# Optimization experiments

Measured on AMD Instinct MI355X. Metric: run time of the kernel, lower is better.

The kernel has to match this reference:

```python
import jax, jax.numpy as jnp
import numpy as np
import math

E = 65536        # neighbor pairs (edges)
NAT = 2048       # atoms
NRAD = 24        # radial basis size
ZETA = [1, 2, 3, 4]
NCOMP = len(ZETA) + 1  # radial components: one 2-body + one per zeta
RCUT = 6.0
NELEM = 94       # one-hot element encoding size
EMB = 16         # species embedding dim


def _tables():
    """Static lxlylz enumeration per zeta: triples with lx+ly+lz = n, n in 0..z,
    multinomial/binomial normalization and (-1)^n lambda sign."""
    f = np.vectorize(math.factorial)
    tabs = []
    for z in ZETA:
        L = []
        for n in range(z + 1):
            for lx in range(n + 1):
                for ly in range(n - lx + 1):
                    L.append((lx, ly, n - lx - ly))
        L = np.array(L, np.int64)              # [K,3]
        nsum = L.sum(1)                        # [K]
        fact_lxlylz = f(L[:, 0]) * f(L[:, 1]) * f(L[:, 2])
        # (nfact/fact_lxlylz) * z!/((z-n)! n!) = z! / ((z-n)! * lx!ly!lz!)
        fact_norm = math.factorial(z) / (f(z - nsum) * fact_lxlylz)
        lam = (-1.0) ** nsum
        tabs.append((jnp.asarray(L, jnp.float32),
                     jnp.asarray(fact_norm, jnp.float32),
                     jnp.asarray(lam, jnp.float32)))
    return tabs

TABS = _tables()


def _forward(rij, Wr1, br1, Wr2, br2, Ws1, bs1, Ws2, bs2,
             Wa1, ba1, Wa2, ba2, Wa3, ba3, first_atom_idx, species_idx):
    nat = species_idx.shape[0]
    r = jnp.linalg.norm(rij, axis=1)                       # [E]
    u = rij / r[:, None]                                   # [E,3] unit vectors
    fc = 0.5 * (jnp.cos(jnp.pi * jnp.minimum(r, RCUT) / RCUT) + 1.0)
    centers = jnp.linspace(0.0, RCUT, NRAD, dtype=jnp.float32)
    width = RCUT / NRAD
    basis = jnp.exp(-((r[:, None] - centers) ** 2) / (2.0 * width * width)) * fc[:, None]  # [E,NRAD]
    # learned radial functions -> [E, NRAD, NCOMP]
    h = jax.nn.silu(basis @ Wr1 + br1)
    radial = jax.nn.silu(h @ Wr2 + br2).reshape(-1, NRAD, NCOMP)
    seg = first_atom_idx
    # two-body descriptor
    feats = [jax.ops.segment_sum(radial[:, :, 0], seg, num_segments=nat)]  # [nat,NRAD]
    for iz, z in enumerate(ZETA):
        L, fnorm, lam = TABS[iz]
        # g_ij over lxlylz combos: prod of powers of unit-vector components
        g_ij = jnp.prod((u[:, None, :] + 1e-12) ** L[None, :, :], axis=-1) * fnorm  # [E,K]
        g = jnp.einsum('er,ek->erk', radial[:, :, iz + 1], g_ij)                    # [E,NRAD,K]
        gi = jax.ops.segment_sum(g, seg, num_segments=nat)                          # [nat,NRAD,K]
        g2 = gi * gi
        norm = 2.0 ** (1.0 - z)
        feats.append(jnp.sum(g2, axis=-1) * norm)          # lambda = +1
        feats.append(jnp.sum(g2 * lam, axis=-1) * norm)    # lambda = -1
    feat = jnp.concatenate(feats, axis=1)                  # [nat, NRAD*(1+2*nzeta)]
    # species embedding and correlation
    onehot = jax.nn.one_hot(species_idx, NELEM, dtype=feat.dtype)
    emb = jax.nn.silu(onehot @ Ws1 + bs1) @ Ws2 + bs2      # [nat,EMB]
    x = (feat[:, :, None] * emb[:, None, :]).reshape(nat, -1)  # [nat, F*EMB]
    h = jax.nn.silu(x @ Wa1 + ba1)
    h = jax.nn.silu(h @ Wa2 + ba2)
    e = h @ Wa3 + ba3                                      # [nat,1] atomic energies
    return jnp.sum(e)                                      # total energy


def setup_inputs() -> dict:
    key = jax.random.key(0)
    ks = jax.random.split(key, 12)
    def w(k, shp):
        return jax.random.normal(k, shp, jnp.float32) / np.float32(np.sqrt(shp[0]))
    F = NRAD * (1 + 2 * len(ZETA)) * EMB  # 3456
    return {
        "rij": jax.random.normal(ks[0], (E, 3), jnp.float32) * 2.0,
        "Wr1": w(ks[1], (NRAD, 64)), "br1": jnp.zeros((64,), jnp.float32),
        "Wr2": w(ks[2], (64, NCOMP * NRAD)), "br2": jnp.zeros((NCOMP * NRAD,), jnp.float32),
        "Ws1": w(ks[3], (NELEM, 32)), "bs1": jnp.zeros((32,), jnp.float32),
        "Ws2": w(ks[4], (32, EMB)), "bs2": jnp.zeros((EMB,), jnp.float32),
        "Wa1": w(ks[5], (F, 256)), "ba1": jnp.zeros((256,), jnp.float32),
        "Wa2": w(ks[6], (256, 128)), "ba2": jnp.zeros((128,), jnp.float32),
        "Wa3": w(ks[7], (128, 1)), "ba3": jnp.zeros((1,), jnp.float32),
        "first_atom_idx": jnp.sort(jax.random.randint(ks[8], (E,), 0, NAT)),
        "species_idx": jax.random.randint(ks[9], (NAT,), 0, NELEM),
    }


def reference(rij, Wr1, br1, Wr2, br2, Ws1, bs1, Ws2, bs2,
              Wa1, ba1, Wa2, ba2, Wa3, ba3, first_atom_idx, species_idx):
    return _forward(rij, Wr1, br1, Wr2, br2, Ws1, bs1, Ws2, bs2,
                    Wa1, ba1, Wa2, ba2, Wa3, ba3, first_atom_idx, species_idx)
```

## Files before the change

### kernel.cpp

```cpp
#include <hip/hip_runtime.h>
#include <math.h>

#define KTOT 69
#define NRADC 24
#define NFEAT 216
#define NELEMC 94
#define EMBC 16
#define H1C 256
#define H2C 128
#define CE 16
#define EPR 20
#define KGN 18
#define GSTR 84
#define GISTR 76

__device__ __constant__ int c_lx[KTOT] = {
  0,0,0,1,
  0,0,0,1,0,0,0,1,1,2,
  0,0,0,1,0,0,0,1,1,2,0,0,0,0,1,1,1,2,2,3,
  0,0,0,1,0,0,0,1,1,2,0,0,0,0,1,1,1,2,2,3,0,0,0,0,0,1,1,1,1,2,2,2,3,3,4};
__device__ __constant__ int c_ly[KTOT] = {
  0,0,1,0,
  0,0,1,0,0,1,2,0,1,0,
  0,0,1,0,0,1,2,0,1,0,0,1,2,3,0,1,2,0,1,0,
  0,0,1,0,0,1,2,0,1,0,0,1,2,3,0,1,2,0,1,0,0,1,2,3,4,0,1,2,3,0,1,2,0,1,0};
__device__ __constant__ int c_lz[KTOT] = {
  0,1,0,0,
  0,1,0,0,2,1,0,1,0,0,
  0,1,0,0,2,1,0,1,0,0,3,2,1,0,2,1,0,1,0,0,
  0,1,0,0,2,1,0,1,0,0,3,2,1,0,2,1,0,1,0,0,4,3,2,1,0,3,2,1,0,2,1,0,1,0,0};
__device__ __constant__ float c_fn[KTOT] = {
  1,1,1,1,
  1,2,2,2,1,2,1,2,2,1,
  1,3,3,3,3,6,3,6,6,3,1,3,3,1,3,6,3,3,3,1,
  1,4,4,4,6,12,6,12,12,6,4,12,12,4,12,24,12,12,12,4,
  1,4,6,4,1,4,12,12,4,6,12,6,4,4,1};
__device__ __constant__ float c_lam[KTOT] = {
  1,-1,-1,-1,
  1,-1,-1,-1,1,1,1,1,1,1,
  1,-1,-1,-1,1,1,1,1,1,1,-1,-1,-1,-1,-1,-1,-1,-1,-1,-1,
  1,-1,-1,-1,1,1,1,1,1,1,-1,-1,-1,-1,-1,-1,-1,-1,-1,-1,
  1,1,1,1,1,1,1,1,1,1,1,1,1,1,1};
__device__ __constant__ int c_k0[4] = {0,4,14,34};
__device__ __constant__ int c_kn[4] = {4,10,20,35};
__device__ __constant__ float c_zn[4] = {1.0f, 0.5f, 0.25f, 0.125f};
__device__ __constant__ int c_zidg[KGN] = {0, 1,1,1, 2,2,2,2,2, 3,3,3,3,3,3,3,3,3};

__device__ __forceinline__ float silu(float x) { return x / (1.0f + expf(-x)); }
__device__ __forceinline__ float4 silu4(float4 v) {
  v.x = silu(v.x); v.y = silu(v.y); v.z = silu(v.z); v.w = silu(v.w); return v;
}
__device__ __forceinline__ void fma4(float4& a, float s, const float4 w) {
  a.x += s * w.x; a.y += s * w.y; a.z += s * w.z; a.w += s * w.w;
}
__device__ __forceinline__ void fma44(float4& a, const float4 x, const float4 y) {
  a.x += x.x * y.x; a.y += x.y * y.y; a.z += x.z * y.z; a.w += x.w * y.w;
}
__device__ __forceinline__ float hsum4(const float4 v) { return (v.x + v.y) + (v.z + v.w); }
__device__ __forceinline__ float powsel(int l, float p, float p2, float p3, float p4) {
  float v = 1.0f;
  v = l >= 1 ? p : v;
  v = l >= 2 ? p2 : v;
  v = l >= 3 ? p3 : v;
  v = l >= 4 ? p4 : v;
  return v;
}

__global__ __launch_bounds__(256) void k_prep(
    const int* __restrict__ fai, const int* __restrict__ spc,
    const float* __restrict__ Ws1, const float* __restrict__ bs1,
    const float* __restrict__ Ws2, const float* __restrict__ bs2,
    const float* __restrict__ Wa1,
    int* __restrict__ bounds, int* __restrict__ order,
    float* __restrict__ B, int E, int nat, int nbB) {
  const int blk = blockIdx.x;
  const int tid = threadIdx.x;
  __shared__ float s_hh[NELEMC * 32];
  __shared__ float s_emb[NELEMC * EMBC];
  __shared__ int s_cnt[NELEMC];
  __shared__ int s_off[NELEMC];

  if (blk < nbB) {
    int e = blk * 256 + tid;
    if (e < E) {
      int f = fai[e];
      int fp = (e == 0) ? -1 : fai[e - 1];
      for (int a = fp + 1; a <= f; ++a) bounds[a] = e;
      if (e == E - 1)
        for (int a = f + 1; a <= nat; ++a) bounds[a] = E;
    }
  } else if (blk == nbB) {
    for (int i = tid; i < NELEMC; i += 256) s_cnt[i] = 0;
    __syncthreads();
    for (int a = tid; a < nat; a += 256) atomicAdd(&s_cnt[spc[a]], 1);
    __syncthreads();
    if (tid == 0) {
      int run = 0;
      for (int s = 0; s < NELEMC; ++s) { s_off[s] = run; run += s_cnt[s]; }
    }
    __syncthreads();
    for (int a = tid; a < nat; a += 256) {
      int pos = atomicAdd(&s_off[spc[a]], 1);
      order[pos] = a;
    }
  } else {
    const int i = blk - nbB - 1;
    const int o = tid;
    for (int idx = tid; idx < NELEMC * 32; idx += 256) {
      int s = idx >> 5, c = idx & 31;
      s_hh[idx] = silu(Ws1[s * 32 + c] + bs1[c]);
    }
    __syncthreads();
    for (int idx = tid; idx < NELEMC * EMBC; idx += 256) {
      int s = idx >> 4, j = idx & 15;
      float acc = bs2[j];
      #pragma unroll
      for (int c = 0; c < 32; ++c) acc += s_hh[s * 32 + c] * Ws2[c * EMBC + j];
      s_emb[idx] = acc;
    }
    __syncthreads();
    float w[EMBC];
    #pragma unroll
    for (int j = 0; j < EMBC; ++j) w[j] = Wa1[(size_t)(i * EMBC + j) * H1C + o];
    for (int s = 0; s < NELEMC; ++s) {
      float acc = 0.0f;
      #pragma unroll
      for (int j = 0; j < EMBC; ++j) acc += s_emb[s * EMBC + j] * w[j];
      B[((size_t)s * NFEAT + i) * H1C + o] = acc;
    }
  }
}

template <int NQ>
__device__ __forceinline__ void edge_l2(
    const float* __restrict__ s_h, const float* __restrict__ Wr2,
    const float* __restrict__ br2, float4* __restrict__ radial4,
    int lane, int og, int ebase, int E) {
  float4 a0[NQ], a1[NQ];
  const float4* b2 = (const float4*)(br2 + og * 32);
  #pragma unroll
  for (int q = 0; q < NQ; ++q) { a0[q] = b2[q]; a1[q] = b2[q]; }
  #pragma unroll 2
  for (int j = 0; j < 64; ++j) {
    float h0 = s_h[lane * 65 + j];
    float h1 = s_h[(lane + 64) * 65 + j];
    const float4* w = (const float4*)(Wr2 + j * 120 + og * 32);
    #pragma unroll
    for (int q = 0; q < NQ; ++q) {
      float4 wq = w[q];
      fma4(a0[q], h0, wq);
      fma4(a1[q], h1, wq);
    }
  }
  const int e0 = ebase + lane, e1 = e0 + 64;
  if (e0 < E) {
    #pragma unroll
    for (int q = 0; q < NQ; ++q) radial4[e0 * 30 + og * 8 + q] = silu4(a0[q]);
  }
  if (e1 < E) {
    #pragma unroll
    for (int q = 0; q < NQ; ++q) radial4[e1 * 30 + og * 8 + q] = silu4(a1[q]);
  }
}

__global__ __launch_bounds__(256) void k_edge(
    const float* __restrict__ rij,
    const float* __restrict__ Wr1, const float* __restrict__ br1,
    const float* __restrict__ Wr2, const float* __restrict__ br2,
    float4* __restrict__ radial4, int E) {
  __shared__ float s_bas[128 * 25];
  __shared__ float s_h[128 * 65];
  const int tid = threadIdx.x;
  const int lane = tid & 63;
  const int og = __builtin_amdgcn_readfirstlane(tid >> 6);
  const int ebase = blockIdx.x * 128;

  {
    const int ehh = og >> 1;
    const int m0 = (og & 1) * 12;
    const int el = ehh * 64 + lane;
    const int eg = ebase + el;
    float x = 0.0f, y = 0.0f, z = 0.0f;
    const bool ev = eg < E;
    if (ev) { x = rij[3 * eg]; y = rij[3 * eg + 1]; z = rij[3 * eg + 2]; }
    float r = sqrtf(x * x + y * y + z * z);
    float fcv = ev ? 0.5f * (cosf(3.14159265358979323846f * fminf(r, 6.0f) *
                                  (1.0f / 6.0f)) + 1.0f)
                   : 0.0f;
    #pragma unroll
    for (int t = 0; t < 12; ++t) {
      int m = m0 + t;
      float d = r - (6.0f / 23.0f) * (float)m;
      s_bas[el * 25 + m] = expf(-8.0f * d * d) * fcv;
    }
  }
  __syncthreads();

  {
    const float4* b1 = (const float4*)(br1 + og * 16);
    float4 c0[4], c1[4];
    #pragma unroll
    for (int q = 0; q < 4; ++q) { c0[q] = b1[q]; c1[q] = b1[q]; }
    #pragma unroll 4
    for (int m = 0; m < NRADC; ++m) {
      float bA = s_bas[lane * 25 + m];
      float bB = s_bas[(lane + 64) * 25 + m];
      const float4* w = (const float4*)(Wr1 + m * 64 + og * 16);
      #pragma unroll
      for (int q = 0; q < 4; ++q) {
        float4 wq = w[q];
        fma4(c0[q], bA, wq);
        fma4(c1[q], bB, wq);
      }
    }
    #pragma unroll
    for (int q = 0; q < 4; ++q) {
      float4 v0 = silu4(c0[q]), v1 = silu4(c1[q]);
      int b0 = lane * 65 + og * 16 + 4 * q;
      int b1o = (lane + 64) * 65 + og * 16 + 4 * q;
      s_h[b0 + 0] = v0.x; s_h[b0 + 1] = v0.y; s_h[b0 + 2] = v0.z; s_h[b0 + 3] = v0.w;
      s_h[b1o + 0] = v1.x; s_h[b1o + 1] = v1.y; s_h[b1o + 2] = v1.z; s_h[b1o + 3] = v1.w;
    }
  }
  __syncthreads();

  if (og < 3) edge_l2<8>(s_h, Wr2, br2, radial4, lane, og, ebase, E);
  else        edge_l2<6>(s_h, Wr2, br2, radial4, lane, og, ebase, E);
}

__global__ __launch_bounds__(256) void k_atom(
    const float* __restrict__ rij,
    const float4* __restrict__ radial4,
    const int* __restrict__ bounds,
    float* __restrict__ feat, int E) {
  const int a = blockIdx.x;
  const int tid = threadIdx.x;
  __shared__ __align__(16) float s_radT[120 * EPR];
  __shared__ __align__(16) float s_gijT[KGN * GSTR];
  __shared__ __align__(16) float s_gi[NRADC * GISTR];
  __shared__ float s_feat[NFEAT];

  const int start = bounds[a];
  const int end = bounds[a + 1];

  const int e = tid & 15;
  const int sub = tid >> 4;

  const bool is_tile = tid < 216;
  const int eh = (tid < 216) ? (tid / 108) : 0;
  const int tile = (tid < 216) ? (tid % 108) : 0;
  const int rg = tile % 6;
  const int kg = tile / 6;
  const int comp0 = rg * 20 + 1 + c_zidg[kg];
  const bool is_2b = (tid >= 216 && tid < 240);
  const int rad2b = tid - 216;

  const int kstart = sub < 5 ? sub * 5 : 25 + (sub - 5) * 4;
  const int kcnt = sub < 5 ? 5 : 4;
  int t_pk[5], t_addr[5]; float t_fn[5];
  #pragma unroll
  for (int t = 0; t < 5; ++t) {
    int k = (t < kcnt) ? kstart + t : 0;
    t_pk[t] = c_lx[k] | (c_ly[k] << 8) | (c_lz[k] << 16);
    t_fn[t] = c_fn[k];
    int prow = k + (k < 14 ? 0 : 2);
    t_addr[t] = (prow >> 2) * GSTR + (prow & 3) * EPR + e;
  }

  const int pe0 = tid / 30, pc0 = tid - pe0 * 30;
  const int pe1 = (tid + 256) / 30, pc1 = (tid + 256) - pe1 * 30;

  if (tid < 60) {
    int rr = tid / EPR, ec = tid % EPR;
    int fkg = rr < 2 ? 3 : 17;
    int fj = rr < 2 ? 2 + rr : 3;
    s_gijT[fkg * GSTR + fj * EPR + ec] = 0.0f;
  }

  float4 acc[4][4];
  #pragma unroll
  for (int i = 0; i < 4; ++i)
    #pragma unroll
    for (int j = 0; j < 4; ++j) acc[i][j] = make_float4(0, 0, 0, 0);
  float4 acc2b = make_float4(0, 0, 0, 0);

  float4 pfA, pfB;
  float rx, ry, rz;
  auto prefetch = [&](int c0) {
    int lim = (end - c0) * 30;
    pfA = make_float4(0, 0, 0, 0);
    pfB = make_float4(0, 0, 0, 0);
    if (tid < lim) pfA = radial4[(size_t)c0 * 30 + tid];
    if (tid < 224 && tid + 256 < lim) pfB = radial4[(size_t)c0 * 30 + 256 + tid];
    int eg = c0 + e;
    rx = 0.0f; ry = 0.0f; rz = 0.0f;
    if (eg < end) { rx = rij[3 * eg]; ry = rij[3 * eg + 1]; rz = rij[3 * eg + 2]; }
  };
  prefetch(start);

  for (int c0 = start; c0 < end; c0 += CE) {
    __syncthreads();
    {
      int c = pc0 * 4;
      s_radT[(c + 0) * EPR + pe0] = pfA.x;
      s_radT[(c + 1) * EPR + pe0] = pfA.y;
      s_radT[(c + 2) * EPR + pe0] = pfA.z;
      s_radT[(c + 3) * EPR + pe0] = pfA.w;
      if (tid < 224) {
        int c2 = pc1 * 4;
        s_radT[(c2 + 0) * EPR + pe1] = pfB.x;
        s_radT[(c2 + 1) * EPR + pe1] = pfB.y;
        s_radT[(c2 + 2) * EPR + pe1] = pfB.z;
        s_radT[(c2 + 3) * EPR + pe1] = pfB.w;
      }
    }
    {
      const bool ev = (c0 + e) < end;
      float r = sqrtf(rx * rx + ry * ry + rz * rz);
      float inv = 1.0f / r;
      float px = rx * inv + 1e-12f, py = ry * inv + 1e-12f, pz = rz * inv + 1e-12f;
      float p2x = px * px, p3x = p2x * px, p4x = p2x * p2x;
      float p2y = py * py, p3y = p2y * py, p4y = p2y * p2y;
      float p2z = pz * pz, p3z = p2z * pz, p4z = p2z * p2z;
      #pragma unroll
      for (int t = 0; t < 5; ++t) {
        if (t < kcnt) {
          int pk = t_pk[t];
          float g = powsel(pk & 0xff, px, p2x, p3x, p4x) *
                    powsel((pk >> 8) & 0xff, py, p2y, p3y, p4y) *
                    powsel(pk >> 16, pz, p2z, p3z, p4z) * t_fn[t];
          s_gijT[t_addr[t]] = ev ? g : 0.0f;
        }
      }
    }
    __syncthreads();
    prefetch(c0 + CE);
    if (is_tile) {
      #pragma unroll
      for (int s = 0; s < 2; ++s) {
        int e0 = eh * 8 + s * 4;
        float4 gg[4];
        #pragma unroll
        for (int j = 0; j < 4; ++j)
          gg[j] = *(const float4*)&s_gijT[kg * GSTR + j * EPR + e0];
        #pragma unroll
        for (int i = 0; i < 4; ++i) {
          float4 rr = *(const float4*)&s_radT[(comp0 + 5 * i) * EPR + e0];
          #pragma unroll
          for (int j = 0; j < 4; ++j) fma44(acc[i][j], rr, gg[j]);
        }
      }
    }
    if (is_2b) {
      #pragma unroll
      for (int e0 = 0; e0 < 16; e0 += 4) {
        float4 v = *(const float4*)&s_radT[(rad2b * 5) * EPR + e0];
        acc2b.x += v.x; acc2b.y += v.y; acc2b.z += v.z; acc2b.w += v.w;
      }
    }
  }

  float4 hs[4];
  #pragma unroll
  for (int i = 0; i < 4; ++i)
    hs[i] = make_float4(hsum4(acc[i][0]), hsum4(acc[i][1]),
                        hsum4(acc[i][2]), hsum4(acc[i][3]));
  __syncthreads();
  if (is_tile && eh == 0) {
    #pragma unroll
    for (int i = 0; i < 4; ++i)
      *(float4*)&s_gi[(rg * 4 + i) * GISTR + kg * 4] = hs[i];
  }
  if (is_2b) s_feat[rad2b] = hsum4(acc2b);
  __syncthreads();
  if (is_tile && eh == 1) {
    #pragma unroll
    for (int i = 0; i < 4; ++i) {
      float4 v = *(const float4*)&s_gi[(rg * 4 + i) * GISTR + kg * 4];
      v.x += hs[i].x; v.y += hs[i].y; v.z += hs[i].z; v.w += hs[i].w;
      *(float4*)&s_gi[(rg * 4 + i) * GISTR + kg * 4] = v;
    }
  }
  __syncthreads();

  if (tid < 192) {
    int zb = tid / NRADC;
    int rad = tid - zb * NRADC;
    int z = zb >> 1;
    bool neg = zb & 1;
    int k0 = c_k0[z], kn = c_kn[z];
    float s = 0.0f;
    for (int k = k0; k < k0 + kn; ++k) {
      int prow = k + (k < 14 ? 0 : 2);
      float g = s_gi[rad * GISTR + prow];
      float g2 = g * g;
      s += neg ? g2 * c_lam[k] : g2;
    }
    s_feat[NRADC + zb * NRADC + rad] = s * c_zn[z];
  }
  __syncthreads();
  if (tid < NFEAT) feat[(size_t)a * NFEAT + tid] = s_feat[tid];
}

__global__ __launch_bounds__(256) void k_mlp(
    const float* __restrict__ feat, const float* __restrict__ B,
    const float* __restrict__ ba1, const float* __restrict__ Wa2,
    const float* __restrict__ ba2, const float* __restrict__ Wa3,
    const float* __restrict__ ba3, const int* __restrict__ order,
    const int* __restrict__ sp, float* __restrict__ e_out, int nat) {
  const int nb = gridDim.x;
  int blk = blockIdx.x;
  if ((nb & 7) == 0) blk = (blockIdx.x & 7) * (nb >> 3) + (blockIdx.x >> 3);
  const int w = threadIdx.x >> 6;
  const int l = threadIdx.x & 63;
  const int rank = blk * 4 + w;
  if (rank >= nat) return;
  const int a = order[rank];
  const int s = sp[a];
  __shared__ __align__(16) float s_f[4][220];
  __shared__ __align__(16) float s_h1[4][260];

  if (l < 54) {
    float4 v = *(const float4*)(feat + (size_t)a * NFEAT + l * 4);
    *(float4*)&s_f[w][l * 4] = v;
  }
  __syncthreads();
  {
    float4 a0 = *(const float4*)(ba1 + l * 4);
    float4 a1 = make_float4(0, 0, 0, 0);
    const float* Bp = B + (size_t)s * NFEAT * H1C + l * 4;
    #pragma unroll 8
    for (int i = 0; i < NFEAT; i += 2) {
      float4 b0 = *(const float4*)(Bp + (size_t)i * H1C);
      float4 b1 = *(const float4*)(Bp + (size_t)(i + 1) * H1C);
      fma4(a0, s_f[w][i], b0);
      fma4(a1, s_f[w][i + 1], b1);
    }
    a0.x += a1.x; a0.y += a1.y; a0.z += a1.z; a0.w += a1.w;
    *(float4*)&s_h1[w][l * 4] = silu4(a0);
  }
  __syncthreads();
  {
    float a0 = ba2[2 * l], a1 = ba2[2 * l + 1];
    #pragma unroll 8
    for (int j = 0; j < H1C; ++j) {
      float hv = s_h1[w][j];
      float2 wv = *(const float2*)(Wa2 + j * H2C + 2 * l);
      a0 += hv * wv.x;
      a1 += hv * wv.y;
    }
    float2 w3 = *(const float2*)(Wa3 + 2 * l);
    float part = silu(a0) * w3.x + silu(a1) * w3.y;
    #pragma unroll
    for (int o = 32; o; o >>= 1) part += __shfl_down(part, o, 64);
    if (l == 0) e_out[a] = part + ba3[0];
  }
}

__global__ void k_reduce(const float* __restrict__ e_in, float* __restrict__ out, int nat) {
  int t = threadIdx.x;
  double acc = 0.0;
  for (int i = t; i < nat; i += 256) acc += (double)e_in[i];
  for (int o = 32; o; o >>= 1) acc += __shfl_down(acc, o, 64);
  __shared__ double s_par[4];
  if ((t & 63) == 0) s_par[t >> 6] = acc;
  __syncthreads();
  if (t == 0) out[0] = (float)(s_par[0] + s_par[1] + s_par[2] + s_par[3]);
}

extern "C" void kernel_launch(void* const* d_in, const int* in_sizes, int n_in,
                              void* d_out, int out_size, void* d_ws, size_t ws_size,
                              hipStream_t stream) {
  const float* rij = (const float*)d_in[0];
  const float* Wr1 = (const float*)d_in[1];
  const float* br1 = (const float*)d_in[2];
  const float* Wr2 = (const float*)d_in[3];
  const float* br2 = (const float*)d_in[4];
  const float* Ws1 = (const float*)d_in[5];
  const float* bs1 = (const float*)d_in[6];
  const float* Ws2 = (const float*)d_in[7];
  const float* bs2 = (const float*)d_in[8];
  const float* Wa1 = (const float*)d_in[9];
  const float* ba1 = (const float*)d_in[10];
  const float* Wa2 = (const float*)d_in[11];
  const float* ba2 = (const float*)d_in[12];
  const float* Wa3 = (const float*)d_in[13];
  const float* ba3 = (const float*)d_in[14];
  const int* fai = (const int*)d_in[15];
  const int* spc = (const int*)d_in[16];

  const int E = in_sizes[0] / 3;
  const int nat = in_sizes[16];

  float* ws = (float*)d_ws;
  size_t off = 0;
  float* radial = ws + off; off += (size_t)E * 120;
  float* feat = ws + off;  off += (size_t)nat * NFEAT;
  float* Bm = ws + off;    off += (size_t)NELEMC * NFEAT * H1C;
  float* e_ws = ws + off;  off += (size_t)nat;
  int* order = (int*)(ws + off); off += (size_t)nat;
  int* bounds = (int*)(ws + off);

  const int nbB = (E + 255) / 256;
  k_prep<<<nbB + 1 + NFEAT, 256, 0, stream>>>(fai, spc, Ws1, bs1, Ws2, bs2, Wa1,
                                              bounds, order, Bm, E, nat, nbB);
  k_edge<<<(E + 127) / 128, 256, 0, stream>>>(rij, Wr1, br1, Wr2, br2,
                                              (float4*)radial, E);
  k_atom<<<nat, 256, 0, stream>>>(rij, (const float4*)radial, bounds, feat, E);
  k_mlp<<<(nat + 3) / 4, 256, 0, stream>>>(feat, Bm, ba1, Wa2, ba2, Wa3, ba3,
                                           order, spc, e_ws, nat);
  k_reduce<<<1, 256, 0, stream>>>(e_ws, (float*)d_out, nat);
}
```

Measured before the change: 212.2 us.

## Split species-table prep across more blocks and use one atom per MLP block

The species-projected first-layer table build is now split four ways over species chunks per feature row. This quadruples the prep block count and shrinks per-block serial work and shared memory. The atom MLP now gives each atom a full 256-thread block, one output neuron per thread, instead of four atoms per block with float4 lanes. This raises parallelism and occupancy but loses the vectorised loads and creates 4x more blocks, with a block-level reduction through shared memory.

```diff
diff --git a/kernel.cpp b/kernel.cpp
--- a/kernel.cpp
+++ b/kernel.cpp
@@ -75,8 +75,8 @@
     float* __restrict__ B, int E, int nat, int nbB) {
   const int blk = blockIdx.x;
   const int tid = threadIdx.x;
-  __shared__ float s_hh[NELEMC * 32];
-  __shared__ float s_emb[NELEMC * EMBC];
+  __shared__ float s_hh[24 * 32];
+  __shared__ float s_emb[24 * EMBC];
   __shared__ int s_cnt[NELEMC];
   __shared__ int s_off[NELEMC];
 
@@ -104,14 +104,17 @@
       order[pos] = a;
     }
   } else {
-    const int i = blk - nbB - 1;
+    const int bi = blk - nbB - 1;
+    const int i = bi >> 2;
+    const int sc0 = (bi & 3) * 24;
+    const int scn = min(NELEMC, sc0 + 24) - sc0;
     const int o = tid;
-    for (int idx = tid; idx < NELEMC * 32; idx += 256) {
+    for (int idx = tid; idx < scn * 32; idx += 256) {
       int s = idx >> 5, c = idx & 31;
-      s_hh[idx] = silu(Ws1[s * 32 + c] + bs1[c]);
-    }
-    __syncthreads();
-    for (int idx = tid; idx < NELEMC * EMBC; idx += 256) {
+      s_hh[idx] = silu(Ws1[(sc0 + s) * 32 + c] + bs1[c]);
+    }
+    __syncthreads();
+    for (int idx = tid; idx < scn * EMBC; idx += 256) {
       int s = idx >> 4, j = idx & 15;
       float acc = bs2[j];
       #pragma unroll
@@ -122,11 +125,11 @@
     float w[EMBC];
     #pragma unroll
     for (int j = 0; j < EMBC; ++j) w[j] = Wa1[(size_t)(i * EMBC + j) * H1C + o];
-    for (int s = 0; s < NELEMC; ++s) {
+    for (int s = 0; s < scn; ++s) {
       float acc = 0.0f;
       #pragma unroll
       for (int j = 0; j < EMBC; ++j) acc += s_emb[s * EMBC + j] * w[j];
-      B[((size_t)s * NFEAT + i) * H1C + o] = acc;
+      B[((size_t)(sc0 + s) * NFEAT + i) * H1C + o] = acc;
     }
   }
 }
@@ -411,50 +414,41 @@
   const int nb = gridDim.x;
   int blk = blockIdx.x;
   if ((nb & 7) == 0) blk = (blockIdx.x & 7) * (nb >> 3) + (blockIdx.x >> 3);
-  const int w = threadIdx.x >> 6;
-  const int l = threadIdx.x & 63;
-  const int rank = blk * 4 + w;
-  if (rank >= nat) return;
-  const int a = order[rank];
+  const int a = order[blk];
   const int s = sp[a];
-  __shared__ __align__(16) float s_f[4][220];
-  __shared__ __align__(16) float s_h1[4][260];
-
-  if (l < 54) {
-    float4 v = *(const float4*)(feat + (size_t)a * NFEAT + l * 4);
-    *(float4*)&s_f[w][l * 4] = v;
-  }
+  const int o = threadIdx.x;
+  __shared__ __align__(16) float s_f[NFEAT];
+  __shared__ __align__(16) float s_h1[H1C];
+  __shared__ float s_red[2];
+
+  if (o < 54)
+    *(float4*)&s_f[o * 4] = *(const float4*)(feat + (size_t)a * NFEAT + o * 4);
   __syncthreads();
   {
-    float4 a0 = *(const float4*)(ba1 + l * 4);
-    float4 a1 = make_float4(0, 0, 0, 0);
-    const float* Bp = B + (size_t)s * NFEAT * H1C + l * 4;
+    float a0 = ba1[o], a1 = 0.0f;
+    const float* Bp = B + (size_t)s * NFEAT * H1C + o;
     #pragma unroll 8
     for (int i = 0; i < NFEAT; i += 2) {
-      float4 b0 = *(const float4*)(Bp + (size_t)i * H1C);
-      float4 b1 = *(const float4*)(Bp + (size_t)(i + 1) * H1C);
-      fma4(a0, s_f[w][i], b0);
-      fma4(a1, s_f[w][i + 1], b1);
-    }
-    a0.x += a1.x; a0.y += a1.y; a0.z += a1.z; a0.w += a1.w;
-    *(float4*)&s_h1[w][l * 4] = silu4(a0);
-  }
-  __syncthreads();
-  {
-    float a0 = ba2[2 * l], a1 = ba2[2 * l + 1];
+      a0 += s_f[i] * Bp[(size_t)i * H1C];
+      a1 += s_f[i + 1] * Bp[(size_t)(i + 1) * H1C];
+    }
+    s_h1[o] = silu(a0 + a1);
+  }
+  __syncthreads();
+  if (o < H2C) {
+    float a0 = ba2[o], a1 = 0.0f;
     #pragma unroll 8
-    for (int j = 0; j < H1C; ++j) {
-      float hv = s_h1[w][j];
-      float2 wv = *(const float2*)(Wa2 + j * H2C + 2 * l);
-      a0 += hv * wv.x;
-      a1 += hv * wv.y;
-    }
-    float2 w3 = *(const float2*)(Wa3 + 2 * l);
-    float part = silu(a0) * w3.x + silu(a1) * w3.y;
-    #pragma unroll
-    for (int o = 32; o; o >>= 1) part += __shfl_down(part, o, 64);
-    if (l == 0) e_out[a] = part + ba3[0];
-  }
+    for (int j = 0; j < H1C; j += 2) {
+      a0 += s_h1[j] * Wa2[j * H2C + o];
+      a1 += s_h1[j + 1] * Wa2[(j + 1) * H2C + o];
+    }
+    float part = silu(a0 + a1) * Wa3[o];
+    #pragma unroll
+    for (int d = 32; d; d >>= 1) part += __shfl_down(part, d, 64);
+    if ((o & 63) == 0) s_red[o >> 6] = part;
+  }
+  __syncthreads();
+  if (o == 0) e_out[a] = s_red[0] + s_red[1] + ba3[0];
 }
 
 __global__ void k_reduce(const float* __restrict__ e_in, float* __restrict__ out, int nat) {
@@ -502,12 +496,13 @@
   int* bounds = (int*)(ws + off);
 
   const int nbB = (E + 255) / 256;
-  k_prep<<<nbB + 1 + NFEAT, 256, 0, stream>>>(fai, spc, Ws1, bs1, Ws2, bs2, Wa1,
-                                              bounds, order, Bm, E, nat, nbB);
+  k_prep<<<nbB + 1 + NFEAT * 4, 256, 0, stream>>>(fai, spc, Ws1, bs1, Ws2, bs2,
+                                                  Wa1, bounds, order, Bm, E, nat,
+                                                  nbB);
   k_edge<<<(E + 127) / 128, 256, 0, stream>>>(rij, Wr1, br1, Wr2, br2,
                                               (float4*)radial, E);
   k_atom<<<nat, 256, 0, stream>>>(rij, (const float4*)radial, bounds, feat, E);
-  k_mlp<<<(nat + 3) / 4, 256, 0, stream>>>(feat, Bm, ba1, Wa2, ba2, Wa3, ba3,
-                                           order, spc, e_ws, nat);
+  k_mlp<<<nat, 256, 0, stream>>>(feat, Bm, ba1, Wa2, ba2, Wa3, ba3,
+                                 order, spc, e_ws, nat);
   k_reduce<<<1, 256, 0, stream>>>(e_ws, (float*)d_out, nat);
 }
```

New measurement: 206.5 us. 2.7% less time.
